# Kernel optimization log

Measured on AMD Instinct MI355X. Metric: run time of the kernel, lower is better.

Reference implementation:

```python
import jax, jax.numpy as jnp
import numpy as np

N = 50000          # nodes
E = 800000         # edges (avg degree 16)
IN, HID, OUT = 128, 128, 64
LAMBDA_MAX = 2.0   # DGL default convention for scaled Laplacian (re_norm = 2/lambda_max = 1)


def setup_inputs() -> dict:
    key = jax.random.key(0)
    k1, k2, k3, k4, k5 = jax.random.split(key, 5)
    features = jax.random.normal(k1, (N, IN), dtype=jnp.float32)
    src = jax.random.randint(k2, (E,), 0, N)
    dst = jax.random.randint(k3, (E,), 0, N)
    # ChebConv(k=2) linear: Linear(2*in, out), torch default uniform init
    s1 = 1.0 / np.sqrt(2 * IN)
    W1 = jax.random.uniform(k4, (2 * IN, HID), jnp.float32, -s1, s1)
    b1 = jnp.zeros((HID,), jnp.float32)
    s2 = 1.0 / np.sqrt(2 * HID)
    W2 = jax.random.uniform(k5, (2 * HID, OUT), jnp.float32, -s2, s2)
    b2 = jnp.zeros((OUT,), jnp.float32)
    return {"features": features, "src": src, "dst": dst,
            "W1": W1, "b1": b1, "W2": W2, "b2": b2}


def _cheb_conv(x, src, dst, d_invsqrt, W, b, re_norm):
    msg = (x * d_invsqrt)[src]                                   # [E, d]
    h = jax.ops.segment_sum(msg, dst, num_segments=N) * d_invsqrt  # [N, d]
    # X_1 = L_tilde X_0 = -re_norm * A_hat X + (re_norm - 1) * X
    x1 = -re_norm * h + x * (re_norm - 1.0)
    xt = jnp.concatenate([x, x1], axis=1)                        # [N, 2d]
    return xt @ W + b


def reference(features, src, dst, W1, b1, W2, b2):
    deg = jax.ops.segment_sum(jnp.ones((E,), jnp.float32), dst, num_segments=N)
    d_invsqrt = jnp.power(jnp.clip(deg, 1.0, None), -0.5)[:, None]  # [N,1]
    re_norm = 2.0 / LAMBDA_MAX
    h = _cheb_conv(features, src, dst, d_invsqrt, W1, b1, re_norm)
    # dropout omitted (eval mode)
    h = _cheb_conv(h, src, dst, d_invsqrt, W2, b2, re_norm)
    return h
```

## Files before the change

kernel.cpp:

```cpp
#include <hip/hip_runtime.h>

#define IN_DIM  128

typedef __bf16 bf16x8 __attribute__((ext_vector_type(8)));
typedef float  f32x4  __attribute__((ext_vector_type(4)));

static inline size_t align256(size_t x) { return (x + 255) & ~size_t(255); }

__device__ __forceinline__ ushort f2b1(float f) {
    union { float f; uint u; } c; c.f = f;
    uint u = c.u;
    uint r = (u + 0x7FFFu + ((u >> 16) & 1u)) >> 16;
    return (ushort)r;
}
__device__ __forceinline__ float lo_bf(uint v) {
    union { uint u; float f; } c; c.u = v << 16; return c.f;
}
__device__ __forceinline__ float hi_bf(uint v) {
    union { uint u; float f; } c; c.u = v & 0xffff0000u; return c.f;
}


__global__ void zero_kernel(int4* __restrict__ p, int n16) {
    int i = blockIdx.x * blockDim.x + threadIdx.x;
    if (i < n16) p[i] = make_int4(0, 0, 0, 0);
}

__global__ void hist_kernel(const int* __restrict__ dst, int* __restrict__ deg,
                            int* __restrict__ rank, int E) {
    int e = blockIdx.x * blockDim.x + threadIdx.x;
    if (e < E) rank[e] = atomicAdd(&deg[dst[e]], 1);
}

__global__ __launch_bounds__(256) void scan_blocks(const int* __restrict__ deg,
                                                   int* __restrict__ pre,
                                                   int* __restrict__ bsum, int n) {
    __shared__ int sh[256];
    int t = threadIdx.x;
    int base = blockIdx.x * 1024 + t * 4;
    int v0 = 0, v1 = 0, v2 = 0, v3 = 0;
    if (base + 3 < n) {
        int4 v = *reinterpret_cast<const int4*>(deg + base);
        v0 = v.x; v1 = v.y; v2 = v.z; v3 = v.w;
    } else {
        if (base     < n) v0 = deg[base];
        if (base + 1 < n) v1 = deg[base + 1];
        if (base + 2 < n) v2 = deg[base + 2];
        if (base + 3 < n) v3 = deg[base + 3];
    }
    int s = v0 + v1 + v2 + v3;
    sh[t] = s;
    __syncthreads();
    for (int off = 1; off < 256; off <<= 1) {
        int x = (t >= off) ? sh[t - off] : 0;
        __syncthreads();
        sh[t] += x;
        __syncthreads();
    }
    int excl = sh[t] - s;
    if (t == 255) bsum[blockIdx.x] = sh[255];
    if (base     < n) pre[base]     = excl;
    if (base + 1 < n) pre[base + 1] = excl + v0;
    if (base + 2 < n) pre[base + 2] = excl + v0 + v1;
    if (base + 3 < n) pre[base + 3] = excl + v0 + v1 + v2;
}

__global__ __launch_bounds__(256) void scan_add(
    const int* __restrict__ pre, const int* __restrict__ bsum,
    const int* __restrict__ deg,
    int* __restrict__ rowptr, float* __restrict__ dinv,
    int n, int E, int nb)
{
    __shared__ int sb[64];
    int t = threadIdx.x;
    if (t < 64) {
        int orig = (t < nb) ? bsum[t] : 0;
        int v = orig;
        for (int off = 1; off < 64; off <<= 1) {
            int u = __shfl_up(v, off);
            if (t >= off) v += u;
        }
        sb[t] = v - orig;
    }
    __syncthreads();
    int i = blockIdx.x * blockDim.x + t;
    if (i < n) {
        rowptr[i] = pre[i] + sb[i >> 10];
        int d = deg[i]; if (d < 1) d = 1;
        dinv[i] = rsqrtf((float)d);
    }
    if (i == 0) rowptr[n] = E;
}


template <typename CT>
__global__ __launch_bounds__(256) void phase2_kernel(
    const int* __restrict__ src, const int* __restrict__ dst,
    const int* __restrict__ rowptr, const int* __restrict__ rank,
    CT* __restrict__ col, int E, int fillBlocks,
    const float* __restrict__ feats, const float* __restrict__ dinv,
    ushort* __restrict__ featb, ushort* __restrict__ featbs,
    ushort* __restrict__ z2s, int N, int nbF,
    const float* __restrict__ W1, ushort* __restrict__ W1t,
    const float* __restrict__ W2, ushort* __restrict__ W2ct)
{
    int b = blockIdx.x, t = threadIdx.x;
    if (b < fillBlocks) {
        int e0 = (b * 256 + t) * 4;
        if (e0 + 3 < E) {
            int4 d4 = *reinterpret_cast<const int4*>(dst + e0);
            int4 r4 = *reinterpret_cast<const int4*>(rank + e0);
            int4 s4 = *reinterpret_cast<const int4*>(src + e0);
            col[rowptr[d4.x] + r4.x] = (CT)s4.x;
            col[rowptr[d4.y] + r4.y] = (CT)s4.y;
            col[rowptr[d4.z] + r4.z] = (CT)s4.z;
            col[rowptr[d4.w] + r4.w] = (CT)s4.w;
        } else {
            for (int e = e0; e < E; ++e)
                col[rowptr[dst[e]] + rank[e]] = (CT)src[e];
        }
        return;
    }
    int b2 = b - fillBlocks;
    if (b2 < nbF) {
        size_t i4 = (size_t)b2 * 256 + t;
        if (i4 < (size_t)N * 32) {
            size_t i = i4 * 4;
            float4 v = *reinterpret_cast<const float4*>(feats + i);
            float dv = dinv[i >> 7];
            ushort4 o, os;
            o.x  = f2b1(v.x);      o.y  = f2b1(v.y);      o.z  = f2b1(v.z);      o.w  = f2b1(v.w);
            os.x = f2b1(v.x * dv); os.y = f2b1(v.y * dv); os.z = f2b1(v.z * dv); os.w = f2b1(v.w * dv);
            *reinterpret_cast<ushort4*>(featb  + i) = o;
            *reinterpret_cast<ushort4*>(featbs + i) = os;
        }
    } else if (b2 < nbF + 128) {
        if (b2 == nbF) {
            if (t < 32) *reinterpret_cast<uint2*>(featbs + (size_t)N * 128 + t * 4) = make_uint2(0, 0);
            else if (t < 48) *reinterpret_cast<uint2*>(z2s + (size_t)N * 64 + (t - 32) * 4) = make_uint2(0, 0);
        }
        int i = (b2 - nbF) * 256 + t;
        int k = i >> 7, c = i & 127;
        W1t[(size_t)c * 256 + k] = f2b1(W1[i]);
    } else {
        int i = (b2 - nbF - 128) * 256 + t;
        int c = i >> 7, k = i & 127;
        float v = (c < 64) ? W2[(size_t)k * 64 + c]
                           : W2[(size_t)(128 + k) * 64 + (c - 64)];
        W2ct[(size_t)c * 128 + k] = f2b1(v);
    }
}


template <typename CT>
__global__ __launch_bounds__(256) void agg_sum128(
    const ushort* __restrict__ Xs, const int* __restrict__ rowptr,
    const CT* __restrict__ col, const float* __restrict__ dinv,
    ushort* __restrict__ X1, int nNodes)
{
    int w    = (blockIdx.x * blockDim.x + threadIdx.x) >> 6;
    int lane = threadIdx.x & 63;
    int n0 = w * 2;
    if (n0 >= nNodes) return;
    n0 = __builtin_amdgcn_readfirstlane(n0);
    bool has1 = (n0 + 1) < nNodes;
    int e0a = rowptr[n0];
    int e1a = rowptr[n0 + 1];
    int e1b = has1 ? rowptr[n0 + 2] : e1a;
    float sca = -dinv[n0];
    float scb = -dinv[has1 ? n0 + 1 : n0];
    const uint* Xu = reinterpret_cast<const uint*>(Xs);

    float a0 = 0.f, a1 = 0.f, b0 = 0.f, b1 = 0.f;
    int basea = e0a, baseb = e1a;
    while (basea < e1a || baseb < e1b) {
        int half = lane >> 5, sl = lane & 31;
        int idx = half ? (baseb + sl) : (basea + sl);
        int ee  = half ? e1b : e1a;
        bool okl = idx < ee;
        int cvl = (int)col[okl ? idx : 0];
        int cv  = okl ? cvl : nNodes;
        int cnta = e1a - basea, cntb = e1b - baseb;
        {
            uint va[16], vb[16];
            #pragma unroll
            for (int j = 0; j < 16; ++j) {
                int s0 = __builtin_amdgcn_readlane(cv, j);
                int s1 = __builtin_amdgcn_readlane(cv, 32 + j);
                va[j] = Xu[(uint)(s0 * 64 + lane)];
                vb[j] = Xu[(uint)(s1 * 64 + lane)];
            }
            #pragma unroll
            for (int j = 0; j < 16; ++j) {
                a0 += lo_bf(va[j]); a1 += hi_bf(va[j]);
                b0 += lo_bf(vb[j]); b1 += hi_bf(vb[j]);
            }
        }
        if (cnta > 16 || cntb > 16) {
            uint va[16], vb[16];
            #pragma unroll
            for (int j = 0; j < 16; ++j) {
                int s0 = __builtin_amdgcn_readlane(cv, 16 + j);
                int s1 = __builtin_amdgcn_readlane(cv, 48 + j);
                va[j] = Xu[(uint)(s0 * 64 + lane)];
                vb[j] = Xu[(uint)(s1 * 64 + lane)];
            }
            #pragma unroll
            for (int j = 0; j < 16; ++j) {
                a0 += lo_bf(va[j]); a1 += hi_bf(va[j]);
                b0 += lo_bf(vb[j]); b1 += hi_bf(vb[j]);
            }
        }
        basea += 32; baseb += 32;
    }
    uint oA = (uint)f2b1(a0 * sca) | ((uint)f2b1(a1 * sca) << 16);
    reinterpret_cast<uint*>(X1)[(uint)(n0 * 64 + lane)] = oA;
    if (has1) {
        uint oB = (uint)f2b1(b0 * scb) | ((uint)f2b1(b1 * scb) << 16);
        reinterpret_cast<uint*>(X1)[(uint)((n0 + 1) * 64 + lane)] = oB;
    }
}


template <typename CT>
__global__ __launch_bounds__(256) void agg_sum64(
    const ushort* __restrict__ Zs, const int* __restrict__ rowptr,
    const CT* __restrict__ col, const float* __restrict__ dinv,
    float* __restrict__ Y, int nNodes)
{
    int w    = (blockIdx.x * blockDim.x + threadIdx.x) >> 6;
    int lane = threadIdx.x & 63;
    int n0 = w * 2;
    if (n0 >= nNodes) return;
    n0 = __builtin_amdgcn_readfirstlane(n0);
    bool has1 = (n0 + 1) < nNodes;
    int e0a = rowptr[n0];
    int e1a = rowptr[n0 + 1];
    int e1b = has1 ? rowptr[n0 + 2] : e1a;
    float sca = -dinv[n0];
    float scb = -dinv[has1 ? n0 + 1 : n0];

    float fa = 0.f, fb = 0.f;
    int basea = e0a, baseb = e1a;
    while (basea < e1a || baseb < e1b) {
        int half = lane >> 5, sl = lane & 31;
        int idx = half ? (baseb + sl) : (basea + sl);
        int ee  = half ? e1b : e1a;
        bool okl = idx < ee;
        int cvl = (int)col[okl ? idx : 0];
        int cv  = okl ? cvl : nNodes;
        int cnta = e1a - basea, cntb = e1b - baseb;
        {
            ushort va[16], vb[16];
            #pragma unroll
            for (int j = 0; j < 16; ++j) {
                int s0 = __builtin_amdgcn_readlane(cv, j);
                int s1 = __builtin_amdgcn_readlane(cv, 32 + j);
                va[j] = Zs[(uint)(s0 * 64 + lane)];
                vb[j] = Zs[(uint)(s1 * 64 + lane)];
            }
            #pragma unroll
            for (int j = 0; j < 16; ++j) {
                fa += lo_bf((uint)va[j]);
                fb += lo_bf((uint)vb[j]);
            }
        }
        if (cnta > 16 || cntb > 16) {
            ushort va[16], vb[16];
            #pragma unroll
            for (int j = 0; j < 16; ++j) {
                int s0 = __builtin_amdgcn_readlane(cv, 16 + j);
                int s1 = __builtin_amdgcn_readlane(cv, 48 + j);
                va[j] = Zs[(uint)(s0 * 64 + lane)];
                vb[j] = Zs[(uint)(s1 * 64 + lane)];
            }
            #pragma unroll
            for (int j = 0; j < 16; ++j) {
                fa += lo_bf((uint)va[j]);
                fb += lo_bf((uint)vb[j]);
            }
        }
        basea += 32; baseb += 32;
    }
    Y[(uint)(n0 * 64 + lane)] += fa * sca;
    if (has1)
        Y[(uint)((n0 + 1) * 64 + lane)] += fb * scb;
}


__global__ __launch_bounds__(256) void gemm_mfma1(
    const ushort* __restrict__ XA, const ushort* __restrict__ XB,
    const ushort* __restrict__ Wt, const float* __restrict__ bias,
    ushort* __restrict__ Y, int nNodes)
{
    __shared__ ushort wlds[128 * 256];
    int t = threadIdx.x;

    #pragma unroll
    for (int it = 0; it < 16; ++it) {
        int i = it * 256 + t;
        int c = i >> 5;
        int o = (i & 31) << 4;
        bf16x8 v = *reinterpret_cast<const bf16x8*>(Wt + ((size_t)c << 8) + (o >> 1));
        *reinterpret_cast<bf16x8*>((char*)wlds + ((size_t)c << 9) + (o ^ ((c & 7) << 4))) = v;
    }
    __syncthreads();

    int wave = t >> 6, lane = t & 63;
    int r16 = lane & 15, g = lane >> 4;
    int nodeBase = blockIdx.x * 128 + wave * 32;

    int arow0 = nodeBase + r16;       if (arow0 > nNodes - 1) arow0 = nNodes - 1;
    int arow1 = nodeBase + 16 + r16;  if (arow1 > nNodes - 1) arow1 = nNodes - 1;
    const ushort* pA0 = XA + (size_t)arow0 * 128;
    const ushort* pA1 = XA + (size_t)arow1 * 128;
    const ushort* pB0 = XB + (size_t)arow0 * 128;
    const ushort* pB1 = XB + (size_t)arow1 * 128;

    f32x4 acc0[8], acc1[8];
    #pragma unroll
    for (int i = 0; i < 8; ++i) { acc0[i] = f32x4{0,0,0,0}; acc1[i] = f32x4{0,0,0,0}; }

    #pragma unroll
    for (int kb = 0; kb < 8; ++kb) {
        int kk = (kb & 3) * 32 + g * 8;
        bf16x8 a0 = *reinterpret_cast<const bf16x8*>(((kb < 4) ? pA0 : pB0) + kk);
        bf16x8 a1 = *reinterpret_cast<const bf16x8*>(((kb < 4) ? pA1 : pB1) + kk);
        int o = kb * 64 + g * 16;
        #pragma unroll
        for (int ct = 0; ct < 8; ++ct) {
            int c = ct * 16 + r16;
            bf16x8 b = *reinterpret_cast<const bf16x8*>(
                (const char*)wlds + ((size_t)c << 9) + (o ^ ((c & 7) << 4)));
            acc0[ct] = __builtin_amdgcn_mfma_f32_16x16x32_bf16(a0, b, acc0[ct], 0, 0, 0);
            acc1[ct] = __builtin_amdgcn_mfma_f32_16x16x32_bf16(a1, b, acc1[ct], 0, 0, 0);
        }
    }

    #pragma unroll
    for (int ct = 0; ct < 8; ++ct) {
        float bv = bias[ct * 16 + r16];
        #pragma unroll
        for (int r = 0; r < 4; ++r) {
            int orow0 = nodeBase + g * 4 + r;
            int orow1 = orow0 + 16;
            if (orow0 < nNodes) Y[(size_t)orow0 * 128 + ct * 16 + r16] = f2b1(acc0[ct][r] + bv);
            if (orow1 < nNodes) Y[(size_t)orow1 * 128 + ct * 16 + r16] = f2b1(acc1[ct][r] + bv);
        }
    }
}


__global__ __launch_bounds__(256) void gemm_mfma2(
    const ushort* __restrict__ H1, const ushort* __restrict__ W2ct,
    const float* __restrict__ bias, const float* __restrict__ dinv,
    float* __restrict__ Yout, ushort* __restrict__ Z2, int nNodes)
{
    __shared__ ushort wlds[128 * 128];
    int t = threadIdx.x;

    #pragma unroll
    for (int it = 0; it < 8; ++it) {
        int i = it * 256 + t;
        int c = i >> 4;
        int o = (i & 15) << 4;
        bf16x8 v = *reinterpret_cast<const bf16x8*>(W2ct + ((size_t)c << 7) + (o >> 1));
        *reinterpret_cast<bf16x8*>((char*)wlds + ((size_t)c << 8) + (o ^ ((c & 7) << 4))) = v;
    }
    __syncthreads();

    int wave = t >> 6, lane = t & 63;
    int r16 = lane & 15, g = lane >> 4;
    int nodeBase = blockIdx.x * 128 + wave * 32;

    int arow0 = nodeBase + r16;       if (arow0 > nNodes - 1) arow0 = nNodes - 1;
    int arow1 = nodeBase + 16 + r16;  if (arow1 > nNodes - 1) arow1 = nNodes - 1;
    const ushort* p0 = H1 + (size_t)arow0 * 128;
    const ushort* p1 = H1 + (size_t)arow1 * 128;

    f32x4 acc0[8], acc1[8];
    #pragma unroll
    for (int i = 0; i < 8; ++i) { acc0[i] = f32x4{0,0,0,0}; acc1[i] = f32x4{0,0,0,0}; }

    #pragma unroll
    for (int kb = 0; kb < 4; ++kb) {
        int kk = kb * 32 + g * 8;
        bf16x8 a0 = *reinterpret_cast<const bf16x8*>(p0 + kk);
        bf16x8 a1 = *reinterpret_cast<const bf16x8*>(p1 + kk);
        int o = kb * 64 + g * 16;
        #pragma unroll
        for (int ct = 0; ct < 8; ++ct) {
            int c = ct * 16 + r16;
            bf16x8 b = *reinterpret_cast<const bf16x8*>(
                (const char*)wlds + ((size_t)c << 8) + (o ^ ((c & 7) << 4)));
            acc0[ct] = __builtin_amdgcn_mfma_f32_16x16x32_bf16(a0, b, acc0[ct], 0, 0, 0);
            acc1[ct] = __builtin_amdgcn_mfma_f32_16x16x32_bf16(a1, b, acc1[ct], 0, 0, 0);
        }
    }

    float dv0[4], dv1[4];
    #pragma unroll
    for (int r = 0; r < 4; ++r) {
        int o0 = nodeBase + g * 4 + r;      if (o0 > nNodes - 1) o0 = nNodes - 1;
        int o1 = nodeBase + 16 + g * 4 + r; if (o1 > nNodes - 1) o1 = nNodes - 1;
        dv0[r] = dinv[o0]; dv1[r] = dinv[o1];
    }

    #pragma unroll
    for (int ct = 0; ct < 8; ++ct) {
        float bv = (ct < 4) ? bias[ct * 16 + r16] : 0.f;
        #pragma unroll
        for (int r = 0; r < 4; ++r) {
            int orow0 = nodeBase + g * 4 + r;
            int orow1 = orow0 + 16;
            if (ct < 4) {
                if (orow0 < nNodes) Yout[(size_t)orow0 * 64 + ct * 16 + r16] = acc0[ct][r] + bv;
                if (orow1 < nNodes) Yout[(size_t)orow1 * 64 + ct * 16 + r16] = acc1[ct][r] + bv;
            } else {
                if (orow0 < nNodes) Z2[(size_t)orow0 * 64 + (ct - 4) * 16 + r16] = f2b1(acc0[ct][r] * dv0[r]);
                if (orow1 < nNodes) Z2[(size_t)orow1 * 64 + (ct - 4) * 16 + r16] = f2b1(acc1[ct][r] * dv1[r]);
            }
        }
    }
}


extern "C" void kernel_launch(void* const* d_in, const int* in_sizes, int n_in,
                              void* d_out, int out_size, void* d_ws, size_t ws_size,
                              hipStream_t stream)
{
    const float* feats = (const float*)d_in[0];
    const int*   src   = (const int*)d_in[1];
    const int*   dst   = (const int*)d_in[2];
    const float* W1    = (const float*)d_in[3];
    const float* b1    = (const float*)d_in[4];
    const float* W2    = (const float*)d_in[5];
    const float* b2    = (const float*)d_in[6];
    float* out = (float*)d_out;

    const int N = in_sizes[0] / IN_DIM;
    const int E = in_sizes[1];
    const int NB = (N + 1023) / 1024;

    char* ws = (char*)d_ws;
    size_t off = 0;
    int*    deg    = (int*)(ws + off);    off = align256(off + (size_t)N * 4);
    int*    rowptr = (int*)(ws + off);    off = align256(off + (size_t)(N + 1) * 4);
    int*    pre    = (int*)(ws + off);    off = align256(off + (size_t)N * 4);
    int*    bsum   = (int*)(ws + off);    off = align256(off + (size_t)64 * 4);
    int*    rank   = (int*)(ws + off);    off = align256(off + (size_t)E * 4);
    void*   colv   = (void*)(ws + off);   off = align256(off + (size_t)E * 4);
    float*  dinv   = (float*)(ws + off);  off = align256(off + (size_t)N * 4);
    ushort* featb  = (ushort*)(ws + off); off = align256(off + (size_t)N * 128 * 2);
    ushort* featbs = (ushort*)(ws + off); off = align256(off + (size_t)(N + 1) * 128 * 2);
    ushort* x1b    = (ushort*)(ws + off); off = align256(off + (size_t)N * 128 * 2);
    ushort* h1b    = (ushort*)(ws + off); off = align256(off + (size_t)N * 128 * 2);
    ushort* z2s    = (ushort*)(ws + off); off = align256(off + (size_t)(N + 1) * 64 * 2);
    ushort* W1t    = (ushort*)(ws + off); off = align256(off + (size_t)256 * 128 * 2);
    ushort* W2ct   = (ushort*)(ws + off); off = align256(off + (size_t)128 * 128 * 2);

    const int n16 = (N + 3) / 4;
    zero_kernel<<<(n16 + 255) / 256, 256, 0, stream>>>((int4*)deg, n16);
    hist_kernel<<<(E + 255) / 256, 256, 0, stream>>>(dst, deg, rank, E);
    scan_blocks<<<NB, 256, 0, stream>>>(deg, pre, bsum, N);
    scan_add<<<(N + 255) / 256, 256, 0, stream>>>(pre, bsum, deg, rowptr, dinv, N, E, NB);

    const bool small = (N <= 65535);
    const int fillBlocks = ((E + 3) / 4 + 255) / 256;
    const int nbF = (N * 32 + 255) / 256;
    const int p2Blocks = fillBlocks + nbF + 128 + 64;
    if (small)
        phase2_kernel<ushort><<<p2Blocks, 256, 0, stream>>>(
            src, dst, rowptr, rank, (ushort*)colv, E, fillBlocks,
            feats, dinv, featb, featbs, z2s, N, nbF, W1, W1t, W2, W2ct);
    else
        phase2_kernel<uint><<<p2Blocks, 256, 0, stream>>>(
            src, dst, rowptr, rank, (uint*)colv, E, fillBlocks,
            feats, dinv, featb, featbs, z2s, N, nbF, W1, W1t, W2, W2ct);

    const int nPairWaves = (N + 1) / 2;
    const int aggBlocks = (nPairWaves * 64 + 255) / 256;
    const int gemmBlocks = (N + 127) / 128;

    if (small)
        agg_sum128<ushort><<<aggBlocks, 256, 0, stream>>>(featbs, rowptr, (const ushort*)colv, dinv, x1b, N);
    else
        agg_sum128<uint><<<aggBlocks, 256, 0, stream>>>(featbs, rowptr, (const uint*)colv, dinv, x1b, N);
    gemm_mfma1<<<gemmBlocks, 256, 0, stream>>>(featb, x1b, W1t, b1, h1b, N);

    gemm_mfma2<<<gemmBlocks, 256, 0, stream>>>(h1b, W2ct, b2, dinv, out, z2s, N);
    if (small)
        agg_sum64<ushort><<<aggBlocks, 256, 0, stream>>>(z2s, rowptr, (const ushort*)colv, dinv, out, N);
    else
        agg_sum64<uint><<<aggBlocks, 256, 0, stream>>>(z2s, rowptr, (const uint*)colv, dinv, out, N);
}
```

Measured before the change: 142.9 us.

## Fuse graph preprocessing kernels into one persistent kernel with grid barriers

Merges the histogram, block scan, scan-add and CSR fill/feature-conversion kernels into a single persistent kernel of 512 blocks, separated by software grid-wide barriers built on an atomic counter. The aim is to remove several kernel launch gaps and their tails in the preprocessing stage. In exchange, work runs in grid-stride loops over fewer blocks. The spin barriers assume all 512 blocks are co-resident; if they are not, the kernel deadlocks.

```diff
diff --git a/kernel.cpp b/kernel.cpp
--- a/kernel.cpp
+++ b/kernel.cpp
@@ -1,6 +1,7 @@
 #include <hip/hip_runtime.h>
 
 #define IN_DIM  128
+#define PREP_G  512
 
 typedef __bf16 bf16x8 __attribute__((ext_vector_type(8)));
 typedef float  f32x4  __attribute__((ext_vector_type(4)));
@@ -21,60 +22,82 @@
 }
 
 
-__global__ void zero_kernel(int4* __restrict__ p, int n16) {
+__global__ void init_kernel(int4* __restrict__ deg4, int n16, int* __restrict__ bar) {
     int i = blockIdx.x * blockDim.x + threadIdx.x;
-    if (i < n16) p[i] = make_int4(0, 0, 0, 0);
-}
-
-__global__ void hist_kernel(const int* __restrict__ dst, int* __restrict__ deg,
-                            int* __restrict__ rank, int E) {
-    int e = blockIdx.x * blockDim.x + threadIdx.x;
-    if (e < E) rank[e] = atomicAdd(&deg[dst[e]], 1);
-}
-
-__global__ __launch_bounds__(256) void scan_blocks(const int* __restrict__ deg,
-                                                   int* __restrict__ pre,
-                                                   int* __restrict__ bsum, int n) {
+    if (i < n16) deg4[i] = make_int4(0, 0, 0, 0);
+    if (i == 0) *bar = 0;
+}
+
+
+__device__ __forceinline__ void grid_bar(int* __restrict__ bar, int target) {
+    __syncthreads();
+    if (threadIdx.x == 0) {
+        __threadfence();
+        atomicAdd(bar, 1);
+        while (__hip_atomic_load(bar, __ATOMIC_ACQUIRE, __HIP_MEMORY_SCOPE_AGENT) < target)
+            __builtin_amdgcn_s_sleep(8);
+        __threadfence();
+    }
+    __syncthreads();
+}
+
+
+template <typename CT>
+__global__ __launch_bounds__(256) void prep_fused(
+    const int* __restrict__ src, const int* __restrict__ dst, int E,
+    int* __restrict__ deg, int* __restrict__ rank, int* __restrict__ pre,
+    int* __restrict__ bsum, int* __restrict__ rowptr, float* __restrict__ dinv,
+    CT* __restrict__ col,
+    const float* __restrict__ feats, ushort* __restrict__ featb,
+    ushort* __restrict__ featbs, ushort* __restrict__ z2s, int N,
+    const float* __restrict__ W1, ushort* __restrict__ W1t,
+    const float* __restrict__ W2, ushort* __restrict__ W2ct,
+    int NB, int* __restrict__ bar)
+{
     __shared__ int sh[256];
-    int t = threadIdx.x;
-    int base = blockIdx.x * 1024 + t * 4;
-    int v0 = 0, v1 = 0, v2 = 0, v3 = 0;
-    if (base + 3 < n) {
-        int4 v = *reinterpret_cast<const int4*>(deg + base);
-        v0 = v.x; v1 = v.y; v2 = v.z; v3 = v.w;
-    } else {
-        if (base     < n) v0 = deg[base];
-        if (base + 1 < n) v1 = deg[base + 1];
-        if (base + 2 < n) v2 = deg[base + 2];
-        if (base + 3 < n) v3 = deg[base + 3];
-    }
-    int s = v0 + v1 + v2 + v3;
-    sh[t] = s;
-    __syncthreads();
-    for (int off = 1; off < 256; off <<= 1) {
-        int x = (t >= off) ? sh[t - off] : 0;
+    __shared__ int sb[64];
+    const int t = threadIdx.x;
+    const int G = gridDim.x;
+    const int gtid = blockIdx.x * 256 + t;
+    const int gstride = G * 256;
+
+    for (int e = gtid; e < E; e += gstride)
+        rank[e] = atomicAdd(&deg[dst[e]], 1);
+    grid_bar(bar, G);
+
+    for (int bi = blockIdx.x; bi < NB; bi += G) {
+        int base = bi * 1024 + t * 4;
+        int v0 = 0, v1 = 0, v2 = 0, v3 = 0;
+        if (base + 3 < N) {
+            int4 v = *reinterpret_cast<const int4*>(deg + base);
+            v0 = v.x; v1 = v.y; v2 = v.z; v3 = v.w;
+        } else {
+            if (base     < N) v0 = deg[base];
+            if (base + 1 < N) v1 = deg[base + 1];
+            if (base + 2 < N) v2 = deg[base + 2];
+            if (base + 3 < N) v3 = deg[base + 3];
+        }
+        int s = v0 + v1 + v2 + v3;
         __syncthreads();
-        sh[t] += x;
+        sh[t] = s;
         __syncthreads();
-    }
-    int excl = sh[t] - s;
-    if (t == 255) bsum[blockIdx.x] = sh[255];
-    if (base     < n) pre[base]     = excl;
-    if (base + 1 < n) pre[base + 1] = excl + v0;
-    if (base + 2 < n) pre[base + 2] = excl + v0 + v1;
-    if (base + 3 < n) pre[base + 3] = excl + v0 + v1 + v2;
-}
-
-__global__ __launch_bounds__(256) void scan_add(
-    const int* __restrict__ pre, const int* __restrict__ bsum,
-    const int* __restrict__ deg,
-    int* __restrict__ rowptr, float* __restrict__ dinv,
-    int n, int E, int nb)
-{
-    __shared__ int sb[64];
-    int t = threadIdx.x;
+        for (int off = 1; off < 256; off <<= 1) {
+            int x = (t >= off) ? sh[t - off] : 0;
+            __syncthreads();
+            sh[t] += x;
+            __syncthreads();
+        }
+        int excl = sh[t] - s;
+        if (t == 255) bsum[bi] = sh[255];
+        if (base     < N) pre[base]     = excl;
+        if (base + 1 < N) pre[base + 1] = excl + v0;
+        if (base + 2 < N) pre[base + 2] = excl + v0 + v1;
+        if (base + 3 < N) pre[base + 3] = excl + v0 + v1 + v2;
+    }
+    grid_bar(bar, 2 * G);
+
     if (t < 64) {
-        int orig = (t < nb) ? bsum[t] : 0;
+        int orig = (t < NB) ? bsum[t] : 0;
         int v = orig;
         for (int off = 1; off < 64; off <<= 1) {
             int u = __shfl_up(v, off);
@@ -83,71 +106,62 @@
         sb[t] = v - orig;
     }
     __syncthreads();
-    int i = blockIdx.x * blockDim.x + t;
-    if (i < n) {
+    for (int i = gtid; i < N; i += gstride) {
         rowptr[i] = pre[i] + sb[i >> 10];
         int d = deg[i]; if (d < 1) d = 1;
         dinv[i] = rsqrtf((float)d);
     }
-    if (i == 0) rowptr[n] = E;
-}
-
-
-template <typename CT>
-__global__ __launch_bounds__(256) void phase2_kernel(
-    const int* __restrict__ src, const int* __restrict__ dst,
-    const int* __restrict__ rowptr, const int* __restrict__ rank,
-    CT* __restrict__ col, int E, int fillBlocks,
-    const float* __restrict__ feats, const float* __restrict__ dinv,
-    ushort* __restrict__ featb, ushort* __restrict__ featbs,
-    ushort* __restrict__ z2s, int N, int nbF,
-    const float* __restrict__ W1, ushort* __restrict__ W1t,
-    const float* __restrict__ W2, ushort* __restrict__ W2ct)
-{
-    int b = blockIdx.x, t = threadIdx.x;
-    if (b < fillBlocks) {
-        int e0 = (b * 256 + t) * 4;
-        if (e0 + 3 < E) {
-            int4 d4 = *reinterpret_cast<const int4*>(dst + e0);
-            int4 r4 = *reinterpret_cast<const int4*>(rank + e0);
-            int4 s4 = *reinterpret_cast<const int4*>(src + e0);
-            col[rowptr[d4.x] + r4.x] = (CT)s4.x;
-            col[rowptr[d4.y] + r4.y] = (CT)s4.y;
-            col[rowptr[d4.z] + r4.z] = (CT)s4.z;
-            col[rowptr[d4.w] + r4.w] = (CT)s4.w;
+    if (gtid == 0) rowptr[N] = E;
+    grid_bar(bar, 3 * G);
+
+    const int fillBlocks = ((E + 3) / 4 + 255) / 256;
+    const int nbF = (N * 32 + 255) / 256;
+    const int total = fillBlocks + nbF + 128 + 64;
+    for (int b = blockIdx.x; b < total; b += G) {
+        if (b < fillBlocks) {
+            int e0 = (b * 256 + t) * 4;
+            if (e0 + 3 < E) {
+                int4 d4 = *reinterpret_cast<const int4*>(dst + e0);
+                int4 r4 = *reinterpret_cast<const int4*>(rank + e0);
+                int4 s4 = *reinterpret_cast<const int4*>(src + e0);
+                col[rowptr[d4.x] + r4.x] = (CT)s4.x;
+                col[rowptr[d4.y] + r4.y] = (CT)s4.y;
+                col[rowptr[d4.z] + r4.z] = (CT)s4.z;
+                col[rowptr[d4.w] + r4.w] = (CT)s4.w;
+            } else {
+                for (int e = e0; e < E; ++e)
+                    col[rowptr[dst[e]] + rank[e]] = (CT)src[e];
+            }
+            continue;
+        }
+        int b2 = b - fillBlocks;
+        if (b2 < nbF) {
+            size_t i4 = (size_t)b2 * 256 + t;
+            if (i4 < (size_t)N * 32) {
+                size_t i = i4 * 4;
+                float4 v = *reinterpret_cast<const float4*>(feats + i);
+                float dv = dinv[i >> 7];
+                ushort4 o, os;
+                o.x  = f2b1(v.x);      o.y  = f2b1(v.y);      o.z  = f2b1(v.z);      o.w  = f2b1(v.w);
+                os.x = f2b1(v.x * dv); os.y = f2b1(v.y * dv); os.z = f2b1(v.z * dv); os.w = f2b1(v.w * dv);
+                *reinterpret_cast<ushort4*>(featb  + i) = o;
+                *reinterpret_cast<ushort4*>(featbs + i) = os;
+            }
+        } else if (b2 < nbF + 128) {
+            if (b2 == nbF) {
+                if (t < 32) *reinterpret_cast<uint2*>(featbs + (size_t)N * 128 + t * 4) = make_uint2(0, 0);
+                else if (t < 48) *reinterpret_cast<uint2*>(z2s + (size_t)N * 64 + (t - 32) * 4) = make_uint2(0, 0);
+            }
+            int i = (b2 - nbF) * 256 + t;
+            int k = i >> 7, c = i & 127;
+            W1t[(size_t)c * 256 + k] = f2b1(W1[i]);
         } else {
-            for (int e = e0; e < E; ++e)
-                col[rowptr[dst[e]] + rank[e]] = (CT)src[e];
-        }
-        return;
-    }
-    int b2 = b - fillBlocks;
-    if (b2 < nbF) {
-        size_t i4 = (size_t)b2 * 256 + t;
-        if (i4 < (size_t)N * 32) {
-            size_t i = i4 * 4;
-            float4 v = *reinterpret_cast<const float4*>(feats + i);
-            float dv = dinv[i >> 7];
-            ushort4 o, os;
-            o.x  = f2b1(v.x);      o.y  = f2b1(v.y);      o.z  = f2b1(v.z);      o.w  = f2b1(v.w);
-            os.x = f2b1(v.x * dv); os.y = f2b1(v.y * dv); os.z = f2b1(v.z * dv); os.w = f2b1(v.w * dv);
-            *reinterpret_cast<ushort4*>(featb  + i) = o;
-            *reinterpret_cast<ushort4*>(featbs + i) = os;
-        }
-    } else if (b2 < nbF + 128) {
-        if (b2 == nbF) {
-            if (t < 32) *reinterpret_cast<uint2*>(featbs + (size_t)N * 128 + t * 4) = make_uint2(0, 0);
-            else if (t < 48) *reinterpret_cast<uint2*>(z2s + (size_t)N * 64 + (t - 32) * 4) = make_uint2(0, 0);
-        }
-        int i = (b2 - nbF) * 256 + t;
-        int k = i >> 7, c = i & 127;
-        W1t[(size_t)c * 256 + k] = f2b1(W1[i]);
-    } else {
-        int i = (b2 - nbF - 128) * 256 + t;
-        int c = i >> 7, k = i & 127;
-        float v = (c < 64) ? W2[(size_t)k * 64 + c]
-                           : W2[(size_t)(128 + k) * 64 + (c - 64)];
-        W2ct[(size_t)c * 128 + k] = f2b1(v);
+            int i = (b2 - nbF - 128) * 256 + t;
+            int c = i >> 7, k = i & 127;
+            float v = (c < 64) ? W2[(size_t)k * 64 + c]
+                               : W2[(size_t)(128 + k) * 64 + (c - 64)];
+            W2ct[(size_t)c * 128 + k] = f2b1(v);
+        }
     }
 }
 
@@ -448,6 +462,7 @@
     int*    rowptr = (int*)(ws + off);    off = align256(off + (size_t)(N + 1) * 4);
     int*    pre    = (int*)(ws + off);    off = align256(off + (size_t)N * 4);
     int*    bsum   = (int*)(ws + off);    off = align256(off + (size_t)64 * 4);
+    int*    bar    = (int*)(ws + off);    off = align256(off + 256);
     int*    rank   = (int*)(ws + off);    off = align256(off + (size_t)E * 4);
     void*   colv   = (void*)(ws + off);   off = align256(off + (size_t)E * 4);
     float*  dinv   = (float*)(ws + off);  off = align256(off + (size_t)N * 4);
@@ -459,24 +474,19 @@
     ushort* W1t    = (ushort*)(ws + off); off = align256(off + (size_t)256 * 128 * 2);
     ushort* W2ct   = (ushort*)(ws + off); off = align256(off + (size_t)128 * 128 * 2);
 
+    const bool small = (N <= 65535);
+
     const int n16 = (N + 3) / 4;
-    zero_kernel<<<(n16 + 255) / 256, 256, 0, stream>>>((int4*)deg, n16);
-    hist_kernel<<<(E + 255) / 256, 256, 0, stream>>>(dst, deg, rank, E);
-    scan_blocks<<<NB, 256, 0, stream>>>(deg, pre, bsum, N);
-    scan_add<<<(N + 255) / 256, 256, 0, stream>>>(pre, bsum, deg, rowptr, dinv, N, E, NB);
-
-    const bool small = (N <= 65535);
-    const int fillBlocks = ((E + 3) / 4 + 255) / 256;
-    const int nbF = (N * 32 + 255) / 256;
-    const int p2Blocks = fillBlocks + nbF + 128 + 64;
+    init_kernel<<<(n16 + 255) / 256, 256, 0, stream>>>((int4*)deg, n16, bar);
+
     if (small)
-        phase2_kernel<ushort><<<p2Blocks, 256, 0, stream>>>(
-            src, dst, rowptr, rank, (ushort*)colv, E, fillBlocks,
-            feats, dinv, featb, featbs, z2s, N, nbF, W1, W1t, W2, W2ct);
+        prep_fused<ushort><<<PREP_G, 256, 0, stream>>>(
+            src, dst, E, deg, rank, pre, bsum, rowptr, dinv, (ushort*)colv,
+            feats, featb, featbs, z2s, N, W1, W1t, W2, W2ct, NB, bar);
     else
-        phase2_kernel<uint><<<p2Blocks, 256, 0, stream>>>(
-            src, dst, rowptr, rank, (uint*)colv, E, fillBlocks,
-            feats, dinv, featb, featbs, z2s, N, nbF, W1, W1t, W2, W2ct);
+        prep_fused<uint><<<PREP_G, 256, 0, stream>>>(
+            src, dst, E, deg, rank, pre, bsum, rowptr, dinv, (uint*)colv,
+            feats, featb, featbs, z2s, N, W1, W1t, W2, W2ct, NB, bar);
 
     const int nPairWaves = (N + 1) / 2;
     const int aggBlocks = (nPairWaves * 64 + 255) / 256;
```

New measurement: 292.9 us. 105% more time.

## Drop scan_add kernel and unscaled bf16 features; recompute rowptr and dinv inline

Applied to the files above, without the earlier changes.

Removes the scan_add launch and the rowptr and dinv buffers. Each consumer now rebuilds the block-offset prefix with a wave shuffle scan over bsum and computes rsqrt(deg) itself. The unscaled bf16 feature copy is also removed. The first GEMM reads the dinv-scaled features and splits its accumulators into two halves, multiplying the X0 half by sqrt(deg) to undo the scaling. This saves one launch and one N×128 bf16 write and read. In exchange it adds extra shuffle work per wave, and the unscale step may change bf16 rounding accuracy.

```diff
diff --git a/kernel.cpp b/kernel.cpp
--- a/kernel.cpp
+++ b/kernel.cpp
@@ -65,14 +65,20 @@
     if (base + 3 < n) pre[base + 3] = excl + v0 + v1 + v2;
 }
 
-__global__ __launch_bounds__(256) void scan_add(
+
+template <typename CT>
+__global__ __launch_bounds__(256) void phase2_kernel(
+    const int* __restrict__ src, const int* __restrict__ dst,
     const int* __restrict__ pre, const int* __restrict__ bsum,
-    const int* __restrict__ deg,
-    int* __restrict__ rowptr, float* __restrict__ dinv,
-    int n, int E, int nb)
+    const int* __restrict__ deg, const int* __restrict__ rank,
+    CT* __restrict__ col, int E, int fillBlocks,
+    const float* __restrict__ feats,
+    ushort* __restrict__ featbs, ushort* __restrict__ z2s, int N, int nbF, int nb,
+    const float* __restrict__ W1, ushort* __restrict__ W1t,
+    const float* __restrict__ W2, ushort* __restrict__ W2ct)
 {
     __shared__ int sb[64];
-    int t = threadIdx.x;
+    int b = blockIdx.x, t = threadIdx.x;
     if (t < 64) {
         int orig = (t < nb) ? bsum[t] : 0;
         int v = orig;
@@ -83,41 +89,22 @@
         sb[t] = v - orig;
     }
     __syncthreads();
-    int i = blockIdx.x * blockDim.x + t;
-    if (i < n) {
-        rowptr[i] = pre[i] + sb[i >> 10];
-        int d = deg[i]; if (d < 1) d = 1;
-        dinv[i] = rsqrtf((float)d);
-    }
-    if (i == 0) rowptr[n] = E;
-}
-
-
-template <typename CT>
-__global__ __launch_bounds__(256) void phase2_kernel(
-    const int* __restrict__ src, const int* __restrict__ dst,
-    const int* __restrict__ rowptr, const int* __restrict__ rank,
-    CT* __restrict__ col, int E, int fillBlocks,
-    const float* __restrict__ feats, const float* __restrict__ dinv,
-    ushort* __restrict__ featb, ushort* __restrict__ featbs,
-    ushort* __restrict__ z2s, int N, int nbF,
-    const float* __restrict__ W1, ushort* __restrict__ W1t,
-    const float* __restrict__ W2, ushort* __restrict__ W2ct)
-{
-    int b = blockIdx.x, t = threadIdx.x;
+
     if (b < fillBlocks) {
         int e0 = (b * 256 + t) * 4;
         if (e0 + 3 < E) {
             int4 d4 = *reinterpret_cast<const int4*>(dst + e0);
             int4 r4 = *reinterpret_cast<const int4*>(rank + e0);
             int4 s4 = *reinterpret_cast<const int4*>(src + e0);
-            col[rowptr[d4.x] + r4.x] = (CT)s4.x;
-            col[rowptr[d4.y] + r4.y] = (CT)s4.y;
-            col[rowptr[d4.z] + r4.z] = (CT)s4.z;
-            col[rowptr[d4.w] + r4.w] = (CT)s4.w;
+            col[pre[d4.x] + sb[d4.x >> 10] + r4.x] = (CT)s4.x;
+            col[pre[d4.y] + sb[d4.y >> 10] + r4.y] = (CT)s4.y;
+            col[pre[d4.z] + sb[d4.z >> 10] + r4.z] = (CT)s4.z;
+            col[pre[d4.w] + sb[d4.w >> 10] + r4.w] = (CT)s4.w;
         } else {
-            for (int e = e0; e < E; ++e)
-                col[rowptr[dst[e]] + rank[e]] = (CT)src[e];
+            for (int e = e0; e < E; ++e) {
+                int d = dst[e];
+                col[pre[d] + sb[d >> 10] + rank[e]] = (CT)src[e];
+            }
         }
         return;
     }
@@ -127,11 +114,11 @@
         if (i4 < (size_t)N * 32) {
             size_t i = i4 * 4;
             float4 v = *reinterpret_cast<const float4*>(feats + i);
-            float dv = dinv[i >> 7];
-            ushort4 o, os;
-            o.x  = f2b1(v.x);      o.y  = f2b1(v.y);      o.z  = f2b1(v.z);      o.w  = f2b1(v.w);
+            int node = (int)(i4 >> 5);
+            int d = deg[node]; if (d < 1) d = 1;
+            float dv = rsqrtf((float)d);
+            ushort4 os;
             os.x = f2b1(v.x * dv); os.y = f2b1(v.y * dv); os.z = f2b1(v.z * dv); os.w = f2b1(v.w * dv);
-            *reinterpret_cast<ushort4*>(featb  + i) = o;
             *reinterpret_cast<ushort4*>(featbs + i) = os;
         }
     } else if (b2 < nbF + 128) {
@@ -154,21 +141,34 @@
 
 template <typename CT>
 __global__ __launch_bounds__(256) void agg_sum128(
-    const ushort* __restrict__ Xs, const int* __restrict__ rowptr,
-    const CT* __restrict__ col, const float* __restrict__ dinv,
-    ushort* __restrict__ X1, int nNodes)
+    const ushort* __restrict__ Xs, const int* __restrict__ pre,
+    const int* __restrict__ bsum, const int* __restrict__ deg,
+    const CT* __restrict__ col,
+    ushort* __restrict__ X1, int nNodes, int E, int nb)
 {
     int w    = (blockIdx.x * blockDim.x + threadIdx.x) >> 6;
     int lane = threadIdx.x & 63;
     int n0 = w * 2;
     if (n0 >= nNodes) return;
     n0 = __builtin_amdgcn_readfirstlane(n0);
+
+    int orig = (lane < nb) ? bsum[lane] : 0;
+    int sv = orig;
+    for (int off = 1; off < 64; off <<= 1) {
+        int u = __shfl_up(sv, off);
+        if (lane >= off) sv += u;
+    }
+    int sbex = sv - orig;
+
     bool has1 = (n0 + 1) < nNodes;
-    int e0a = rowptr[n0];
-    int e1a = rowptr[n0 + 1];
-    int e1b = has1 ? rowptr[n0 + 2] : e1a;
-    float sca = -dinv[n0];
-    float scb = -dinv[has1 ? n0 + 1 : n0];
+    int e0a = pre[n0] + __shfl(sbex, n0 >> 10);
+    int e1a = (n0 + 1 == nNodes) ? E : pre[n0 + 1] + __shfl(sbex, (n0 + 1) >> 10);
+    int e1b = has1 ? ((n0 + 2 == nNodes) ? E : pre[n0 + 2] + __shfl(sbex, (n0 + 2) >> 10)) : e1a;
+
+    int d0 = deg[n0]; if (d0 < 1) d0 = 1;
+    int d1 = has1 ? deg[n0 + 1] : 1; if (d1 < 1) d1 = 1;
+    float sca = -rsqrtf((float)d0);
+    float scb = -rsqrtf((float)d1);
     const uint* Xu = reinterpret_cast<const uint*>(Xs);
 
     float a0 = 0.f, a1 = 0.f, b0 = 0.f, b1 = 0.f;
@@ -224,21 +224,34 @@
 
 template <typename CT>
 __global__ __launch_bounds__(256) void agg_sum64(
-    const ushort* __restrict__ Zs, const int* __restrict__ rowptr,
-    const CT* __restrict__ col, const float* __restrict__ dinv,
-    float* __restrict__ Y, int nNodes)
+    const ushort* __restrict__ Zs, const int* __restrict__ pre,
+    const int* __restrict__ bsum, const int* __restrict__ deg,
+    const CT* __restrict__ col,
+    float* __restrict__ Y, int nNodes, int E, int nb)
 {
     int w    = (blockIdx.x * blockDim.x + threadIdx.x) >> 6;
     int lane = threadIdx.x & 63;
     int n0 = w * 2;
     if (n0 >= nNodes) return;
     n0 = __builtin_amdgcn_readfirstlane(n0);
+
+    int orig = (lane < nb) ? bsum[lane] : 0;
+    int sv = orig;
+    for (int off = 1; off < 64; off <<= 1) {
+        int u = __shfl_up(sv, off);
+        if (lane >= off) sv += u;
+    }
+    int sbex = sv - orig;
+
     bool has1 = (n0 + 1) < nNodes;
-    int e0a = rowptr[n0];
-    int e1a = rowptr[n0 + 1];
-    int e1b = has1 ? rowptr[n0 + 2] : e1a;
-    float sca = -dinv[n0];
-    float scb = -dinv[has1 ? n0 + 1 : n0];
+    int e0a = pre[n0] + __shfl(sbex, n0 >> 10);
+    int e1a = (n0 + 1 == nNodes) ? E : pre[n0 + 1] + __shfl(sbex, (n0 + 1) >> 10);
+    int e1b = has1 ? ((n0 + 2 == nNodes) ? E : pre[n0 + 2] + __shfl(sbex, (n0 + 2) >> 10)) : e1a;
+
+    int d0 = deg[n0]; if (d0 < 1) d0 = 1;
+    int d1 = has1 ? deg[n0 + 1] : 1; if (d1 < 1) d1 = 1;
+    float sca = -rsqrtf((float)d0);
+    float scb = -rsqrtf((float)d1);
 
     float fa = 0.f, fb = 0.f;
     int basea = e0a, baseb = e1a;
@@ -289,9 +302,9 @@
 
 
 __global__ __launch_bounds__(256) void gemm_mfma1(
-    const ushort* __restrict__ XA, const ushort* __restrict__ XB,
+    const ushort* __restrict__ XS, const ushort* __restrict__ XB,
     const ushort* __restrict__ Wt, const float* __restrict__ bias,
-    ushort* __restrict__ Y, int nNodes)
+    const int* __restrict__ deg, ushort* __restrict__ Y, int nNodes)
 {
     __shared__ ushort wlds[128 * 256];
     int t = threadIdx.x;
@@ -312,29 +325,50 @@
 
     int arow0 = nodeBase + r16;       if (arow0 > nNodes - 1) arow0 = nNodes - 1;
     int arow1 = nodeBase + 16 + r16;  if (arow1 > nNodes - 1) arow1 = nNodes - 1;
-    const ushort* pA0 = XA + (size_t)arow0 * 128;
-    const ushort* pA1 = XA + (size_t)arow1 * 128;
+    const ushort* pA0 = XS + (size_t)arow0 * 128;
+    const ushort* pA1 = XS + (size_t)arow1 * 128;
     const ushort* pB0 = XB + (size_t)arow0 * 128;
     const ushort* pB1 = XB + (size_t)arow1 * 128;
 
-    f32x4 acc0[8], acc1[8];
-    #pragma unroll
-    for (int i = 0; i < 8; ++i) { acc0[i] = f32x4{0,0,0,0}; acc1[i] = f32x4{0,0,0,0}; }
+    f32x4 acc0A[4], acc0B[4], acc1A[4], acc1B[4];
+    f32x4 a0A[8], a0B[8], a1A[8], a1B[8];
+    #pragma unroll
+    for (int i = 0; i < 8; ++i) {
+        a0A[i] = f32x4{0,0,0,0}; a0B[i] = f32x4{0,0,0,0};
+        a1A[i] = f32x4{0,0,0,0}; a1B[i] = f32x4{0,0,0,0};
+    }
+    (void)acc0A; (void)acc0B; (void)acc1A; (void)acc1B;
 
     #pragma unroll
     for (int kb = 0; kb < 8; ++kb) {
         int kk = (kb & 3) * 32 + g * 8;
-        bf16x8 a0 = *reinterpret_cast<const bf16x8*>(((kb < 4) ? pA0 : pB0) + kk);
-        bf16x8 a1 = *reinterpret_cast<const bf16x8*>(((kb < 4) ? pA1 : pB1) + kk);
+        bf16x8 v0 = *reinterpret_cast<const bf16x8*>(((kb < 4) ? pA0 : pB0) + kk);
+        bf16x8 v1 = *reinterpret_cast<const bf16x8*>(((kb < 4) ? pA1 : pB1) + kk);
         int o = kb * 64 + g * 16;
         #pragma unroll
         for (int ct = 0; ct < 8; ++ct) {
             int c = ct * 16 + r16;
-            bf16x8 b = *reinterpret_cast<const bf16x8*>(
+            bf16x8 bfrag = *reinterpret_cast<const bf16x8*>(
                 (const char*)wlds + ((size_t)c << 9) + (o ^ ((c & 7) << 4)));
-            acc0[ct] = __builtin_amdgcn_mfma_f32_16x16x32_bf16(a0, b, acc0[ct], 0, 0, 0);
-            acc1[ct] = __builtin_amdgcn_mfma_f32_16x16x32_bf16(a1, b, acc1[ct], 0, 0, 0);
-        }
+            if (kb < 4) {
+                a0A[ct] = __builtin_amdgcn_mfma_f32_16x16x32_bf16(v0, bfrag, a0A[ct], 0, 0, 0);
+                a1A[ct] = __builtin_amdgcn_mfma_f32_16x16x32_bf16(v1, bfrag, a1A[ct], 0, 0, 0);
+            } else {
+                a0B[ct] = __builtin_amdgcn_mfma_f32_16x16x32_bf16(v0, bfrag, a0B[ct], 0, 0, 0);
+                a1B[ct] = __builtin_amdgcn_mfma_f32_16x16x32_bf16(v1, bfrag, a1B[ct], 0, 0, 0);
+            }
+        }
+    }
+
+    float sq0[4], sq1[4];
+    #pragma unroll
+    for (int r = 0; r < 4; ++r) {
+        int o0 = nodeBase + g * 4 + r;      if (o0 > nNodes - 1) o0 = nNodes - 1;
+        int o1 = nodeBase + 16 + g * 4 + r; if (o1 > nNodes - 1) o1 = nNodes - 1;
+        int d0 = deg[o0]; if (d0 < 1) d0 = 1;
+        int d1 = deg[o1]; if (d1 < 1) d1 = 1;
+        sq0[r] = sqrtf((float)d0);
+        sq1[r] = sqrtf((float)d1);
     }
 
     #pragma unroll
@@ -344,8 +378,8 @@
         for (int r = 0; r < 4; ++r) {
             int orow0 = nodeBase + g * 4 + r;
             int orow1 = orow0 + 16;
-            if (orow0 < nNodes) Y[(size_t)orow0 * 128 + ct * 16 + r16] = f2b1(acc0[ct][r] + bv);
-            if (orow1 < nNodes) Y[(size_t)orow1 * 128 + ct * 16 + r16] = f2b1(acc1[ct][r] + bv);
+            if (orow0 < nNodes) Y[(size_t)orow0 * 128 + ct * 16 + r16] = f2b1(a0A[ct][r] * sq0[r] + a0B[ct][r] + bv);
+            if (orow1 < nNodes) Y[(size_t)orow1 * 128 + ct * 16 + r16] = f2b1(a1A[ct][r] * sq1[r] + a1B[ct][r] + bv);
         }
     }
 }
@@ -353,7 +387,7 @@
 
 __global__ __launch_bounds__(256) void gemm_mfma2(
     const ushort* __restrict__ H1, const ushort* __restrict__ W2ct,
-    const float* __restrict__ bias, const float* __restrict__ dinv,
+    const float* __restrict__ bias, const int* __restrict__ deg,
     float* __restrict__ Yout, ushort* __restrict__ Z2, int nNodes)
 {
     __shared__ ushort wlds[128 * 128];
@@ -385,16 +419,16 @@
     #pragma unroll
     for (int kb = 0; kb < 4; ++kb) {
         int kk = kb * 32 + g * 8;
-        bf16x8 a0 = *reinterpret_cast<const bf16x8*>(p0 + kk);
-        bf16x8 a1 = *reinterpret_cast<const bf16x8*>(p1 + kk);
+        bf16x8 v0 = *reinterpret_cast<const bf16x8*>(p0 + kk);
+        bf16x8 v1 = *reinterpret_cast<const bf16x8*>(p1 + kk);
         int o = kb * 64 + g * 16;
         #pragma unroll
         for (int ct = 0; ct < 8; ++ct) {
             int c = ct * 16 + r16;
-            bf16x8 b = *reinterpret_cast<const bf16x8*>(
+            bf16x8 bfrag = *reinterpret_cast<const bf16x8*>(
                 (const char*)wlds + ((size_t)c << 8) + (o ^ ((c & 7) << 4)));
-            acc0[ct] = __builtin_amdgcn_mfma_f32_16x16x32_bf16(a0, b, acc0[ct], 0, 0, 0);
-            acc1[ct] = __builtin_amdgcn_mfma_f32_16x16x32_bf16(a1, b, acc1[ct], 0, 0, 0);
+            acc0[ct] = __builtin_amdgcn_mfma_f32_16x16x32_bf16(v0, bfrag, acc0[ct], 0, 0, 0);
+            acc1[ct] = __builtin_amdgcn_mfma_f32_16x16x32_bf16(v1, bfrag, acc1[ct], 0, 0, 0);
         }
     }
 
@@ -403,7 +437,10 @@
     for (int r = 0; r < 4; ++r) {
         int o0 = nodeBase + g * 4 + r;      if (o0 > nNodes - 1) o0 = nNodes - 1;
         int o1 = nodeBase + 16 + g * 4 + r; if (o1 > nNodes - 1) o1 = nNodes - 1;
-        dv0[r] = dinv[o0]; dv1[r] = dinv[o1];
+        int d0 = deg[o0]; if (d0 < 1) d0 = 1;
+        int d1 = deg[o1]; if (d1 < 1) d1 = 1;
+        dv0[r] = rsqrtf((float)d0);
+        dv1[r] = rsqrtf((float)d1);
     }
 
     #pragma unroll
@@ -445,13 +482,10 @@
     char* ws = (char*)d_ws;
     size_t off = 0;
     int*    deg    = (int*)(ws + off);    off = align256(off + (size_t)N * 4);
-    int*    rowptr = (int*)(ws + off);    off = align256(off + (size_t)(N + 1) * 4);
     int*    pre    = (int*)(ws + off);    off = align256(off + (size_t)N * 4);
     int*    bsum   = (int*)(ws + off);    off = align256(off + (size_t)64 * 4);
     int*    rank   = (int*)(ws + off);    off = align256(off + (size_t)E * 4);
     void*   colv   = (void*)(ws + off);   off = align256(off + (size_t)E * 4);
-    float*  dinv   = (float*)(ws + off);  off = align256(off + (size_t)N * 4);
-    ushort* featb  = (ushort*)(ws + off); off = align256(off + (size_t)N * 128 * 2);
     ushort* featbs = (ushort*)(ws + off); off = align256(off + (size_t)(N + 1) * 128 * 2);
     ushort* x1b    = (ushort*)(ws + off); off = align256(off + (size_t)N * 128 * 2);
     ushort* h1b    = (ushort*)(ws + off); off = align256(off + (size_t)N * 128 * 2);
@@ -459,38 +493,38 @@
     ushort* W1t    = (ushort*)(ws + off); off = align256(off + (size_t)256 * 128 * 2);
     ushort* W2ct   = (ushort*)(ws + off); off = align256(off + (size_t)128 * 128 * 2);
 
+    const bool small = (N <= 65535);
+
     const int n16 = (N + 3) / 4;
     zero_kernel<<<(n16 + 255) / 256, 256, 0, stream>>>((int4*)deg, n16);
     hist_kernel<<<(E + 255) / 256, 256, 0, stream>>>(dst, deg, rank, E);
     scan_blocks<<<NB, 256, 0, stream>>>(deg, pre, bsum, N);
-    scan_add<<<(N + 255) / 256, 256, 0, stream>>>(pre, bsum, deg, rowptr, dinv, N, E, NB);
-
-    const bool small = (N <= 65535);
+
     const int fillBlocks = ((E + 3) / 4 + 255) / 256;
     const int nbF = (N * 32 + 255) / 256;
     const int p2Blocks = fillBlocks + nbF + 128 + 64;
     if (small)
         phase2_kernel<ushort><<<p2Blocks, 256, 0, stream>>>(
-            src, dst, rowptr, rank, (ushort*)colv, E, fillBlocks,
-            feats, dinv, featb, featbs, z2s, N, nbF, W1, W1t, W2, W2ct);
+            src, dst, pre, bsum, deg, rank, (ushort*)colv, E, fillBlocks,
+            feats, featbs, z2s, N, nbF, NB, W1, W1t, W2, W2ct);
     else
         phase2_kernel<uint><<<p2Blocks, 256, 0, stream>>>(
-            src, dst, rowptr, rank, (uint*)colv, E, fillBlocks,
-            feats, dinv, featb, featbs, z2s, N, nbF, W1, W1t, W2, W2ct);
+            src, dst, pre, bsum, deg, rank, (uint*)colv, E, fillBlocks,
+            feats, featbs, z2s, N, nbF, NB, W1, W1t, W2, W2ct);
 
     const int nPairWaves = (N + 1) / 2;
     const int aggBlocks = (nPairWaves * 64 + 255) / 256;
     const int gemmBlocks = (N + 127) / 128;
 
     if (small)
-        agg_sum128<ushort><<<aggBlocks, 256, 0, stream>>>(featbs, rowptr, (const ushort*)colv, dinv, x1b, N);
+        agg_sum128<ushort><<<aggBlocks, 256, 0, stream>>>(featbs, pre, bsum, deg, (const ushort*)colv, x1b, N, E, NB);
     else
-        agg_sum128<uint><<<aggBlocks, 256, 0, stream>>>(featbs, rowptr, (const uint*)colv, dinv, x1b, N);
-    gemm_mfma1<<<gemmBlocks, 256, 0, stream>>>(featb, x1b, W1t, b1, h1b, N);
-
-    gemm_mfma2<<<gemmBlocks, 256, 0, stream>>>(h1b, W2ct, b2, dinv, out, z2s, N);
+        agg_sum128<uint><<<aggBlocks, 256, 0, stream>>>(featbs, pre, bsum, deg, (const uint*)colv, x1b, N, E, NB);
+    gemm_mfma1<<<gemmBlocks, 256, 0, stream>>>(featbs, x1b, W1t, b1, deg, h1b, N);
+
+    gemm_mfma2<<<gemmBlocks, 256, 0, stream>>>(h1b, W2ct, b2, deg, out, z2s, N);
     if (small)
-        agg_sum64<ushort><<<aggBlocks, 256, 0, stream>>>(z2s, rowptr, (const ushort*)colv, dinv, out, N);
+        agg_sum64<ushort><<<aggBlocks, 256, 0, stream>>>(z2s, pre, bsum, deg, (const ushort*)colv, out, N, E, NB);
     else
-        agg_sum64<uint><<<aggBlocks, 256, 0, stream>>>(z2s, rowptr, (const uint*)colv, dinv, out, N);
-}
+        agg_sum64<uint><<<aggBlocks, 256, 0, stream>>>(z2s, pre, bsum, deg, (const uint*)colv, out, N, E, NB);
+}
```

After: 145.7 us. About the same (+1.9%).
